# Kernel tuning notes

Measured on AMD Instinct MI355X. Metric: run time of the kernel, lower is better.

The kernel has to match this reference:

```python
import jax, jax.numpy as jnp
import numpy as np

N = 50000          # num_nodes
IN_CH = 128
H = 32             # hidden_channels
D = 2              # stalk dimension d (= final_d, add_lp=add_hp=False)
LAYERS = 4
EU = 400000        # undirected edges
E = 2 * EU         # directed edges (both orientations)
OUT = 32


def setup_inputs() -> dict:
    key = jax.random.key(0)
    ks = jax.random.split(key, 12)
    # undirected random graph; directed edge list holds both orientations so that
    # the reverse of directed edge e is e + EU (mod E)
    u = jax.random.randint(ks[0], (EU,), 0, N)
    v = jax.random.randint(ks[1], (EU,), 0, N)
    edge_index = jnp.stack([jnp.concatenate([u, v]), jnp.concatenate([v, u])]).astype(jnp.int64)
    x = jax.random.normal(ks[2], (N, IN_CH), dtype=jnp.float32)
    W1 = jax.random.normal(ks[3], (H * D, IN_CH), dtype=jnp.float32) / np.sqrt(IN_CH)
    b1 = jax.random.normal(ks[4], (H * D,), dtype=jnp.float32) * 0.01
    W_sheaf = jax.random.normal(ks[5], (LAYERS, D, 2 * D * H), dtype=jnp.float32) / np.sqrt(2 * D * H)
    # lin_left initialised to identity in the module; keep near-identity
    W_left = jnp.tile(jnp.eye(D, dtype=jnp.float32), (LAYERS, 1, 1)) \
        + 0.01 * jax.random.normal(ks[6], (LAYERS, D, D), dtype=jnp.float32)
    W_right = jax.random.normal(ks[7], (LAYERS, H, H), dtype=jnp.float32) / np.sqrt(H)
    eps = jnp.zeros((LAYERS, D, 1), dtype=jnp.float32) + 0.01 * jax.random.normal(ks[8], (LAYERS, D, 1), dtype=jnp.float32)
    W2 = jax.random.normal(ks[9], (OUT, D * H), dtype=jnp.float32) / np.sqrt(D * H)
    b2 = jax.random.normal(ks[10], (OUT,), dtype=jnp.float32) * 0.01
    return {"x": x, "edge_index": edge_index, "W1": W1, "b1": b1, "W_sheaf": W_sheaf,
            "W_left": W_left, "W_right": W_right, "eps": eps, "W2": W2, "b2": b2}


def reference(x, edge_index, W1, b1, W_sheaf, W_left, W_right, eps, W2, b2):
    # eval mode: dropouts are no-ops; diagnostic energies/eigsh omitted (no effect on output)
    n = x.shape[0]
    d = W_left.shape[-1]
    h = W_right.shape[-1]
    src, dst = edge_index[0], edge_index[1]
    e = src.shape[0]
    rev = (jnp.arange(e) + e // 2) % e  # reverse directed edge

    x = jax.nn.elu(x @ W1.T + b1)      # [N, d*h]
    x = x.reshape(n * d, h)
    x0 = x

    for l in range(W_left.shape[0]):
        # --- sheaf learner: tanh(Linear([x_i || x_j])), diag maps F: [E, d] ---
        xn = x.reshape(n, d * h)
        feat = jnp.concatenate([xn[src], xn[dst]], axis=-1)   # [E, 2dh]
        F = jnp.tanh(feat @ W_sheaf[l].T)                     # [E, d]
        Fr = F[rev]
        # --- diag sheaf Laplacian (normalised, augmented: D_hat = D + I) ---
        Dg = jax.ops.segment_sum(F * F, src, num_segments=n)  # [N, d] diagonal blocks
        dinv = jax.lax.rsqrt(Dg + 1.0)
        diagw = Dg * dinv * dinv                              # [N, d]
        offw = -F * Fr * dinv[src] * dinv[dst]                # [E, d]
        # --- left weights: view x^T as [h, N, d], mix stalk dim ---
        xt = x.T.reshape(h, n, d) @ W_left[l].T
        x = xt.reshape(h, n * d).T
        # --- right weights ---
        x = x @ W_right[l].T
        # --- spmm: y = L x ---
        x3 = x.reshape(n, d, h)
        y = diagw[:, :, None] * x3 \
            + jax.ops.segment_sum(offw[:, :, None] * x3[dst], src, num_segments=n)
        x = jax.nn.elu(y.reshape(n * d, h))
        # --- epsilon-gated residual ---
        coeff = jnp.tile(1.0 + jnp.tanh(eps[l]), (n, 1))      # [N*d, 1]
        x0 = coeff * x0 - x
        x = x0

    return x.reshape(n, d * h) @ W2.T + b2
```

## Files before the change

kernel.cpp:

```cpp
#include <hip/hip_runtime.h>
#include <math.h>

#define INCH 128
#define DH 64
#define H  32
#define D  2
#define LAYERS 4
#define OUTC 32

typedef __fp16 half4 __attribute__((ext_vector_type(4)));
typedef __fp16 half8 __attribute__((ext_vector_type(8)));
typedef float  f32x4 __attribute__((ext_vector_type(4)));

__device__ __forceinline__ float eluf(float v) { return v > 0.f ? v : expm1f(v); }

__device__ __forceinline__ float ftanh(float x) {
    float xc = fminf(9.0f, fmaxf(-9.0f, x));
    float e2 = __builtin_amdgcn_exp2f(xc * 2.885390081777927f);
    return (e2 - 1.0f) * __builtin_amdgcn_rcpf(e2 + 1.0f);
}

__global__ void k_prep(const float* __restrict__ W1, const float* __restrict__ W2,
                       const float* __restrict__ Wleft, const float* __restrict__ Wright,
                       __fp16* __restrict__ W1h, __fp16* __restrict__ W2h,
                       __fp16* __restrict__ Mlrh) {
    int idx = blockIdx.x * blockDim.x + threadIdx.x;
    if (idx < DH * INCH) {
        W1h[idx] = (__fp16)W1[idx];
    } else if (idx < DH * INCH + OUTC * DH) {
        int i = idx - DH * INCH;
        W2h[i] = (__fp16)W2[i];
    } else if (idx < DH * INCH + OUTC * DH + LAYERS * DH * DH) {
        int i = idx - DH * INCH - OUTC * DH;
        int l = i >> 12;
        int r = i & 4095;
        int row = r >> 6;
        int col = r & 63;
        int sp = row >> 5, c = row & 31;
        int s  = col >> 5, cp = col & 31;
        Mlrh[i] = (__fp16)(Wleft[l * 4 + sp * 2 + s] * Wright[l * 1024 + c * 32 + cp]);
    }
}

__global__ void k_hist(const int* __restrict__ src, int* __restrict__ deg, int E) {
    int e = blockIdx.x * blockDim.x + threadIdx.x;
    if (e < E) atomicAdd(&deg[src[e]], 1);
}

__global__ void k_bsum(const int* __restrict__ deg, int* __restrict__ bsum, int N) {
    int b = blockIdx.x, t = threadIdx.x;
    int lane = t & 63, wid = t >> 6;
    int base = b * 1024 + t * 4;
    int s = 0;
    #pragma unroll
    for (int i = 0; i < 4; ++i) {
        int idx = base + i;
        if (idx < N) s += deg[idx];
    }
    #pragma unroll
    for (int ofs = 32; ofs; ofs >>= 1) s += __shfl_xor(s, ofs);
    __shared__ int ws[4];
    if (lane == 0) ws[wid] = s;
    __syncthreads();
    if (t == 0) bsum[b] = ws[0] + ws[1] + ws[2] + ws[3];
}

__global__ void k_scan_small(int* __restrict__ bsum, int B) {
    int lane = threadIdx.x;
    int carry = 0;
    for (int base = 0; base < B; base += 64) {
        int i = base + lane;
        int v = (i < B) ? bsum[i] : 0;
        int incl = v;
        #pragma unroll
        for (int ofs = 1; ofs < 64; ofs <<= 1) {
            int tt = __shfl_up(incl, ofs);
            if (lane >= ofs) incl += tt;
        }
        if (i < B) bsum[i] = carry + incl - v;
        carry += __shfl(incl, 63);
    }
}

__global__ void k_scan_final(const int* __restrict__ deg, const int* __restrict__ bsum,
                             int* __restrict__ rowptr, int* __restrict__ cur, int N) {
    int b = blockIdx.x, t = threadIdx.x;
    int lane = t & 63, wid = t >> 6;
    int base = b * 1024 + t * 4;
    int v[4];
    int s = 0;
    #pragma unroll
    for (int i = 0; i < 4; ++i) {
        int idx = base + i;
        v[i] = (idx < N) ? deg[idx] : 0;
        s += v[i];
    }
    int incl = s;
    #pragma unroll
    for (int ofs = 1; ofs < 64; ofs <<= 1) {
        int tt = __shfl_up(incl, ofs);
        if (lane >= ofs) incl += tt;
    }
    __shared__ int ws[4];
    if (lane == 63) ws[wid] = incl;
    __syncthreads();
    int woff = 0;
    for (int k = 0; k < wid; ++k) woff += ws[k];
    int excl = bsum[b] + woff + incl - s;
    #pragma unroll
    for (int i = 0; i < 4; ++i) {
        int idx = base + i;
        if (idx < N) { rowptr[idx] = excl; cur[idx] = excl; }
        excl += v[i];
        if (idx == N - 1) rowptr[N] = excl;
    }
}

__global__ void k_scatter(const int* __restrict__ src, const int* __restrict__ dst,
                          int* __restrict__ cur, unsigned short* __restrict__ csr_dst, int E) {
    int e = blockIdx.x * blockDim.x + threadIdx.x;
    if (e >= E) return;
    int pos = atomicAdd(&cur[src[e]], 1);
    csr_dst[pos] = (unsigned short)dst[e];
}


__global__ __launch_bounds__(256) void k_mlp1_pq(const float* __restrict__ xin,
                                                 const __fp16* __restrict__ W1h,
                                                 const float* __restrict__ b1,
                                                 const float* __restrict__ Ws0,
                                                 float* __restrict__ X,
                                                 __fp16* __restrict__ NDh, int N) {
    __shared__ float xs[16 * INCH];
    __shared__ __fp16 wsh[DH * 132];
    __shared__ float xout[16 * DH];
    int t = threadIdx.x;
    int node0 = blockIdx.x * 16;
    for (int i = t; i < 16 * INCH / 4; i += 256) {
        int r = i >> 5, c = (i & 31) * 4;
        int node = node0 + r;
        f32x4 v = (node < N) ? __builtin_nontemporal_load((const f32x4*)(xin + (size_t)node * INCH + c))
                             : (f32x4){0.f, 0.f, 0.f, 0.f};
        *(f32x4*)&xs[r * INCH + c] = v;
    }
    for (int i = t; i < DH * INCH / 4; i += 256) {
        int r = i >> 5, c = (i & 31) * 4;
        *(uint2*)&wsh[r * 132 + c] = ((const uint2*)W1h)[i];
    }
    __syncthreads();
    int w = t >> 6, lane = t & 63;
    int oc0 = w * 16;
    int rr = lane & 15, g = lane >> 4;
    f32x4 acc = {0.f, 0.f, 0.f, 0.f};
    #pragma unroll
    for (int ks = 0; ks < INCH / 16; ++ks) {
        f32x4 xv = *(const f32x4*)&xs[rr * INCH + ks * 16 + g * 4];
        half4 af = {(__fp16)xv.x, (__fp16)xv.y, (__fp16)xv.z, (__fp16)xv.w};
        half4 bf = *(const half4*)&wsh[(oc0 + rr) * 132 + ks * 16 + g * 4];
        acc = __builtin_amdgcn_mfma_f32_16x16x16f16(af, bf, acc, 0, 0, 0);
    }
    int oc = oc0 + rr;
    float bb = b1[oc];
    #pragma unroll
    for (int r = 0; r < 4; ++r) {
        int node = node0 + g * 4 + r;
        float v = eluf(acc[r] + bb);
        xout[(g * 4 + r) * DH + oc] = v;
        if (node < N) X[(size_t)node * DH + oc] = v;
    }
    __syncthreads();
    float wsa = Ws0[lane];
    float wsb = Ws0[64 + lane];
    float wsc = Ws0[128 + lane];
    float wsd = Ws0[192 + lane];
    #pragma unroll
    for (int j = 0; j < 4; ++j) {
        int nl = w * 4 + j;
        int node = node0 + nl;
        float x = xout[nl * DH + lane];
        float p0 = x * wsa, q0 = x * wsb, p1 = x * wsc, q1 = x * wsd;
        #pragma unroll
        for (int ofs = 32; ofs; ofs >>= 1) {
            p0 += __shfl_xor(p0, ofs);
            q0 += __shfl_xor(q0, ofs);
            p1 += __shfl_xor(p1, ofs);
            q1 += __shfl_xor(q1, ofs);
        }
        if (lane == 0 && node < N) {
            half4 pq = {(__fp16)p0, (__fp16)p1, (__fp16)q0, (__fp16)q1};
            *(half4*)(NDh + (size_t)node * 8) = pq;
        }
    }
}

__global__ __launch_bounds__(256) void k_dglr(__fp16* __restrict__ NDh,
                                              const int* __restrict__ rowptr,
                                              const unsigned short* __restrict__ csr_dst,
                                              const float* __restrict__ X,
                                              const __fp16* __restrict__ Mlrh_l,
                                              __fp16* __restrict__ XW0h,
                                              __fp16* __restrict__ XW1h,
                                              int Bdg, int N) {
    __shared__ float xs[16 * DH];
    __shared__ __fp16 mlh[DH * 68];
    if (blockIdx.x < Bdg) {
        int lane = threadIdx.x & 63;
        int widl = threadIdx.x >> 6;
        int nn = lane >> 4, sub = lane & 15;
        int node = blockIdx.x * 16 + widl * 4 + nn;
        if (node >= N) return;
        half4 pqu = *(const half4*)(NDh + (size_t)node * 8);
        float pu0 = (float)pqu[0], pu1 = (float)pqu[1];
        int pos = rowptr[node], end = rowptr[node + 1];
        float sx = 0.f, sy = 0.f;
        for (int i = pos + sub; i < end; i += 16) {
            int v = (int)__builtin_nontemporal_load(csr_dst + i);
            half4 pqv = *(const half4*)(NDh + (size_t)v * 8);
            float fx = ftanh(pu0 + (float)pqv[2]);
            float fy = ftanh(pu1 + (float)pqv[3]);
            sx += fx * fx;
            sy += fy * fy;
        }
        #pragma unroll
        for (int ofs = 8; ofs; ofs >>= 1) {
            sx += __shfl_xor(sx, ofs);
            sy += __shfl_xor(sy, ofs);
        }
        if (sub == 0) {
            float i0 = 1.f / (sx + 1.f), i1 = 1.f / (sy + 1.f);
            half4 gi = {(__fp16)sqrtf(i0), (__fp16)sqrtf(i1), (__fp16)(sx * i0), (__fp16)(sy * i1)};
            *(half4*)(NDh + (size_t)node * 8 + 4) = gi;
        }
        return;
    }
    int t = threadIdx.x;
    int node0 = (blockIdx.x - Bdg) * 16;
    for (int i = t; i < 16 * DH / 4; i += 256) {
        int r = i >> 4, c = (i & 15) * 4;
        int node = node0 + r;
        f32x4 v = (node < N) ? __builtin_nontemporal_load((const f32x4*)(X + (size_t)node * DH + c))
                             : (f32x4){0.f, 0.f, 0.f, 0.f};
        *(f32x4*)&xs[r * DH + c] = v;
    }
    for (int i = t; i < DH * DH / 4; i += 256) {
        int r = i >> 4, c = (i & 15) * 4;
        *(uint2*)&mlh[r * 68 + c] = ((const uint2*)Mlrh_l)[i];
    }
    __syncthreads();
    int w = t >> 6, lane = t & 63;
    int oc0 = w * 16;
    int rr = lane & 15, g = lane >> 4;
    f32x4 acc = {0.f, 0.f, 0.f, 0.f};
    #pragma unroll
    for (int ks = 0; ks < DH / 16; ++ks) {
        f32x4 xv = *(const f32x4*)&xs[rr * DH + ks * 16 + g * 4];
        half4 af = {(__fp16)xv.x, (__fp16)xv.y, (__fp16)xv.z, (__fp16)xv.w};
        half4 bf = *(const half4*)&mlh[(oc0 + rr) * 68 + ks * 16 + g * 4];
        acc = __builtin_amdgcn_mfma_f32_16x16x16f16(af, bf, acc, 0, 0, 0);
    }
    int oc = oc0 + rr;
    int sp = oc >> 5, c = oc & 31;
    __fp16* __restrict__ XWs = sp ? XW1h : XW0h;
    #pragma unroll
    for (int r = 0; r < 4; ++r) {
        int node = node0 + g * 4 + r;
        if (node < N) XWs[(size_t)node * H + c] = (__fp16)acc[r];
    }
}

__global__ __launch_bounds__(256) void k_out(const float* __restrict__ X,
                                             const __fp16* __restrict__ W2h,
                                             const float* __restrict__ b2,
                                             float* __restrict__ out, int N) {
    __shared__ float xs[32 * DH];
    __shared__ __fp16 w2s[OUTC * 68];
    int t = threadIdx.x;
    int node0 = blockIdx.x * 32;
    for (int i = t; i < 32 * DH / 4; i += 256) {
        int r = i >> 4, c = (i & 15) * 4;
        int node = node0 + r;
        f32x4 v = (node < N) ? __builtin_nontemporal_load((const f32x4*)(X + (size_t)node * DH + c))
                             : (f32x4){0.f, 0.f, 0.f, 0.f};
        *(f32x4*)&xs[r * DH + c] = v;
    }
    for (int i = t; i < OUTC * DH / 4; i += 256) {
        int r = i >> 4, c = (i & 15) * 4;
        *(uint2*)&w2s[r * 68 + c] = ((const uint2*)W2h)[i];
    }
    __syncthreads();
    int w = t >> 6, lane = t & 63;
    int nt = w >> 1;
    int oc0 = (w & 1) * 16;
    int rr = lane & 15, g = lane >> 4;
    f32x4 acc = {0.f, 0.f, 0.f, 0.f};
    #pragma unroll
    for (int ks = 0; ks < DH / 16; ++ks) {
        f32x4 xv = *(const f32x4*)&xs[(nt * 16 + rr) * DH + ks * 16 + g * 4];
        half4 af = {(__fp16)xv.x, (__fp16)xv.y, (__fp16)xv.z, (__fp16)xv.w};
        half4 bf = *(const half4*)&w2s[(oc0 + rr) * 68 + ks * 16 + g * 4];
        acc = __builtin_amdgcn_mfma_f32_16x16x16f16(af, bf, acc, 0, 0, 0);
    }
    int oc = oc0 + rr;
    float bb = b2[oc];
    #pragma unroll
    for (int r = 0; r < 4; ++r) {
        int node = node0 + nt * 16 + g * 4 + r;
        if (node < N) out[(size_t)node * OUTC + oc] = acc[r] + bb;
    }
}

__global__ void k_spmm_fin_pq(const __fp16* __restrict__ XW0h, const __fp16* __restrict__ XW1h,
                              const __fp16* __restrict__ NDh, const int* __restrict__ rowptr,
                              const unsigned short* __restrict__ csr_dst,
                              const float* __restrict__ eps_l, const float* __restrict__ Wsn,
                              float* __restrict__ X, __fp16* __restrict__ NDhn, int N) {
    int wid = (blockIdx.x * blockDim.x + threadIdx.x) >> 6;
    int lane = threadIdx.x & 63;
    if (wid >= N) return;
    int q = lane >> 3;
    int m = lane & 7;
    half8 ndu = *(const half8*)(NDh + (size_t)wid * 8);
    float pu0 = (float)ndu[0], pu1 = (float)ndu[1];
    float qu0 = (float)ndu[2], qu1 = (float)ndu[3];
    float dinv0 = (float)ndu[4], dinv1 = (float)ndu[5];
    int pos = rowptr[wid], end = rowptr[wid + 1];

    float a0x = 0.f, a0y = 0.f, a0z = 0.f, a0w = 0.f;
    float a1x = 0.f, a1y = 0.f, a1z = 0.f, a1w = 0.f;

    for (int chunk = pos; chunk < end; chunk += 64) {
        int myidx = chunk + lane;
        int dmy = 0;
        float w0my = 0.f, w1my = 0.f;
        if (myidx < end) {
            dmy = (int)__builtin_nontemporal_load(csr_dst + myidx);
            half8 ndd = *(const half8*)(NDh + (size_t)dmy * 8);
            float ff0 = ftanh(pu0 + (float)ndd[2]), fb0 = ftanh((float)ndd[0] + qu0);
            float ff1 = ftanh(pu1 + (float)ndd[3]), fb1 = ftanh((float)ndd[1] + qu1);
            w0my = -ff0 * fb0 * dinv0 * (float)ndd[4];
            w1my = -ff1 * fb1 * dinv1 * (float)ndd[5];
        }
        int lim = end - chunk; if (lim > 64) lim = 64;
        for (int b = 0; b < lim; b += 8) {
            int sl = b + q;
            int d      = __shfl(dmy, sl);
            float w0e  = __shfl(w0my, sl);
            float w1e  = __shfl(w1my, sl);
            half4 g0 = *(const half4*)(XW0h + (size_t)d * H + m * 4);
            half4 g1 = *(const half4*)(XW1h + (size_t)d * H + m * 4);
            a0x += w0e * (float)g0.x; a0y += w0e * (float)g0.y;
            a0z += w0e * (float)g0.z; a0w += w0e * (float)g0.w;
            a1x += w1e * (float)g1.x; a1y += w1e * (float)g1.y;
            a1z += w1e * (float)g1.z; a1w += w1e * (float)g1.w;
        }
    }
    #pragma unroll
    for (int ofs = 8; ofs <= 32; ofs <<= 1) {
        a0x += __shfl_xor(a0x, ofs); a0y += __shfl_xor(a0y, ofs);
        a0z += __shfl_xor(a0z, ofs); a0w += __shfl_xor(a0w, ofs);
        a1x += __shfl_xor(a1x, ofs); a1y += __shfl_xor(a1y, ofs);
        a1z += __shfl_xor(a1z, ofs); a1w += __shfl_xor(a1w, ofs);
    }
    if (q == 0) {
        float diag0 = (float)ndu[6];
        float diag1 = (float)ndu[7];
        half4 xw0 = *(const half4*)(XW0h + (size_t)wid * H + m * 4);
        half4 xw1 = *(const half4*)(XW1h + (size_t)wid * H + m * 4);
        size_t b0 = (size_t)wid * DH + m * 4;
        size_t b1 = b0 + 32;
        float coeff0 = 1.f + tanhf(eps_l[0]);
        float coeff1 = 1.f + tanhf(eps_l[1]);
        f32x4 xo0 = __builtin_nontemporal_load((const f32x4*)(X + b0));
        f32x4 xo1 = __builtin_nontemporal_load((const f32x4*)(X + b1));
        f32x4 xn0, xn1;
        xn0.x = coeff0 * xo0.x - eluf(diag0 * (float)xw0.x + a0x);
        xn0.y = coeff0 * xo0.y - eluf(diag0 * (float)xw0.y + a0y);
        xn0.z = coeff0 * xo0.z - eluf(diag0 * (float)xw0.z + a0z);
        xn0.w = coeff0 * xo0.w - eluf(diag0 * (float)xw0.w + a0w);
        xn1.x = coeff1 * xo1.x - eluf(diag1 * (float)xw1.x + a1x);
        xn1.y = coeff1 * xo1.y - eluf(diag1 * (float)xw1.y + a1y);
        xn1.z = coeff1 * xo1.z - eluf(diag1 * (float)xw1.z + a1z);
        xn1.w = coeff1 * xo1.w - eluf(diag1 * (float)xw1.w + a1w);
        __builtin_nontemporal_store(xn0, (f32x4*)(X + b0));
        __builtin_nontemporal_store(xn1, (f32x4*)(X + b1));
        if (Wsn) {
            f32x4 wa0 = *(const f32x4*)(Wsn + m * 4);
            f32x4 wa1 = *(const f32x4*)(Wsn + 32 + m * 4);
            f32x4 wb0 = *(const f32x4*)(Wsn + 64 + m * 4);
            f32x4 wb1 = *(const f32x4*)(Wsn + 96 + m * 4);
            f32x4 wc0 = *(const f32x4*)(Wsn + 128 + m * 4);
            f32x4 wc1 = *(const f32x4*)(Wsn + 160 + m * 4);
            f32x4 wd0 = *(const f32x4*)(Wsn + 192 + m * 4);
            f32x4 wd1 = *(const f32x4*)(Wsn + 224 + m * 4);
            float p0 = xn0.x * wa0.x + xn0.y * wa0.y + xn0.z * wa0.z + xn0.w * wa0.w
                     + xn1.x * wa1.x + xn1.y * wa1.y + xn1.z * wa1.z + xn1.w * wa1.w;
            float q0 = xn0.x * wb0.x + xn0.y * wb0.y + xn0.z * wb0.z + xn0.w * wb0.w
                     + xn1.x * wb1.x + xn1.y * wb1.y + xn1.z * wb1.z + xn1.w * wb1.w;
            float p1 = xn0.x * wc0.x + xn0.y * wc0.y + xn0.z * wc0.z + xn0.w * wc0.w
                     + xn1.x * wc1.x + xn1.y * wc1.y + xn1.z * wc1.z + xn1.w * wc1.w;
            float q1 = xn0.x * wd0.x + xn0.y * wd0.y + xn0.z * wd0.z + xn0.w * wd0.w
                     + xn1.x * wd1.x + xn1.y * wd1.y + xn1.z * wd1.z + xn1.w * wd1.w;
            #pragma unroll
            for (int ofs = 1; ofs < 8; ofs <<= 1) {
                p0 += __shfl_xor(p0, ofs);
                q0 += __shfl_xor(q0, ofs);
                p1 += __shfl_xor(p1, ofs);
                q1 += __shfl_xor(q1, ofs);
            }
            if (m == 0) {
                half4 pq = {(__fp16)p0, (__fp16)p1, (__fp16)q0, (__fp16)q1};
                *(half4*)(NDhn + (size_t)wid * 8) = pq;
            }
        }
    }
}

extern "C" void kernel_launch(void* const* d_in, const int* in_sizes, int n_in,
                              void* d_out, int out_size, void* d_ws, size_t ws_size,
                              hipStream_t stream) {
    const float* xin    = (const float*)d_in[0];
    const int*   ei     = (const int*)d_in[1];
    const float* W1     = (const float*)d_in[2];
    const float* b1     = (const float*)d_in[3];
    const float* Wsheaf = (const float*)d_in[4];
    const float* Wleft  = (const float*)d_in[5];
    const float* Wright = (const float*)d_in[6];
    const float* eps    = (const float*)d_in[7];
    const float* W2     = (const float*)d_in[8];
    const float* b2     = (const float*)d_in[9];
    float* out = (float*)d_out;

    int N = in_sizes[0] / INCH;
    int E = in_sizes[1] / 2;
    const int* src = ei;
    const int* dst = ei + E;

    size_t off = 0;
    auto alloc = [&](size_t nbytes) {
        char* p = (char*)d_ws + off;
        off += (nbytes + 255) & ~(size_t)255;
        return p;
    };
    float*          X       = (float*)alloc((size_t)N * DH * 4);
    __fp16*         XW0h    = (__fp16*)alloc((size_t)N * H * 2);
    __fp16*         XW1h    = (__fp16*)alloc((size_t)N * H * 2);
    __fp16*         NDha    = (__fp16*)alloc((size_t)N * 16);
    __fp16*         NDhb    = (__fp16*)alloc((size_t)N * 16);
    int*            deg     = (int*)alloc((size_t)N * 4);
    int*            rowptr  = (int*)alloc(((size_t)N + 1) * 4);
    int*            cur     = (int*)alloc((size_t)N * 4);
    unsigned short* csr_dst = (unsigned short*)alloc((size_t)E * 2);
    int*            bsum    = (int*)alloc(4096);
    __fp16*         W1h     = (__fp16*)alloc((size_t)DH * INCH * 2);
    __fp16*         W2h     = (__fp16*)alloc((size_t)OUTC * DH * 2);
    __fp16*         Mlrh    = (__fp16*)alloc((size_t)LAYERS * DH * DH * 2);

    int B = (N + 1023) / 1024;

    int prep_total = DH * INCH + OUTC * DH + LAYERS * DH * DH;
    k_prep<<<(prep_total + 255) / 256, 256, 0, stream>>>(W1, W2, Wleft, Wright, W1h, W2h, Mlrh);
    hipMemsetAsync(deg, 0, (size_t)N * sizeof(int), stream);
    k_hist<<<(E + 255) / 256, 256, 0, stream>>>(src, deg, E);
    k_bsum<<<B, 256, 0, stream>>>(deg, bsum, N);
    k_scan_small<<<1, 64, 0, stream>>>(bsum, B);
    k_scan_final<<<B, 256, 0, stream>>>(deg, bsum, rowptr, cur, N);
    k_scatter<<<(E + 255) / 256, 256, 0, stream>>>(src, dst, cur, csr_dst, E);

    k_mlp1_pq<<<(N + 15) / 16, 256, 0, stream>>>(xin, W1h, b1, Wsheaf, X, NDha, N);

    __fp16* NDcur = NDha;
    __fp16* NDnext = NDhb;
    int Bdg = (N + 15) / 16;
    int Blr = (N + 15) / 16;
    for (int l = 0; l < LAYERS; ++l) {
        k_dglr<<<Bdg + Blr, 256, 0, stream>>>(NDcur, rowptr, csr_dst, X,
                                              Mlrh + (size_t)l * DH * DH, XW0h, XW1h, Bdg, N);
        const float* Wsn = (l + 1 < LAYERS) ? (Wsheaf + (l + 1) * 2 * INCH) : nullptr;
        k_spmm_fin_pq<<<(N + 3) / 4, 256, 0, stream>>>(XW0h, XW1h, NDcur, rowptr, csr_dst,
                                                       eps + l * 2, Wsn, X, NDnext, N);
        __fp16* tmp = NDcur; NDcur = NDnext; NDnext = tmp;
    }

    k_out<<<(N + 31) / 32, 256, 0, stream>>>(X, W2h, b2, out, N);
}
```

Baseline: 378.4 us.

## Split SpMM per node across two waves, one per stalk dimension

Each node is now handled by two wavefronts, one per stalk component, where before a single wave covered both. Each wave gathers only one XW half and computes one edge weight, which halves per-wave register use and doubles the number of waves in flight for the latency-bound gather. The two partial p/q projections are combined through shared memory after a block barrier. In exchange, edge indices and neighbor metadata are loaded twice and the final step pays a barrier.

```diff
diff --git a/kernel.cpp b/kernel.cpp
--- a/kernel.cpp
+++ b/kernel.cpp
@@ -309,97 +309,79 @@
     }
 }
 
-__global__ void k_spmm_fin_pq(const __fp16* __restrict__ XW0h, const __fp16* __restrict__ XW1h,
-                              const __fp16* __restrict__ NDh, const int* __restrict__ rowptr,
-                              const unsigned short* __restrict__ csr_dst,
-                              const float* __restrict__ eps_l, const float* __restrict__ Wsn,
-                              float* __restrict__ X, __fp16* __restrict__ NDhn, int N) {
-    int wid = (blockIdx.x * blockDim.x + threadIdx.x) >> 6;
+__global__ __launch_bounds__(256) void k_spmm_fin_pq(
+        const __fp16* __restrict__ XW0h, const __fp16* __restrict__ XW1h,
+        const __fp16* __restrict__ NDh, const int* __restrict__ rowptr,
+        const unsigned short* __restrict__ csr_dst,
+        const float* __restrict__ eps_l, const float* __restrict__ Wsn,
+        float* __restrict__ X, __fp16* __restrict__ NDhn, int N) {
+    __shared__ float4 pq_lds[2][2];
+    int wvl = threadIdx.x >> 6;
+    int nl  = wvl >> 1;
+    int st  = wvl & 1;
     int lane = threadIdx.x & 63;
-    if (wid >= N) return;
+    int wid = blockIdx.x * 2 + nl;
+    bool active = wid < N;
     int q = lane >> 3;
     int m = lane & 7;
-    half8 ndu = *(const half8*)(NDh + (size_t)wid * 8);
-    float pu0 = (float)ndu[0], pu1 = (float)ndu[1];
-    float qu0 = (float)ndu[2], qu1 = (float)ndu[3];
-    float dinv0 = (float)ndu[4], dinv1 = (float)ndu[5];
-    int pos = rowptr[wid], end = rowptr[wid + 1];
-
-    float a0x = 0.f, a0y = 0.f, a0z = 0.f, a0w = 0.f;
-    float a1x = 0.f, a1y = 0.f, a1z = 0.f, a1w = 0.f;
-
+    const __fp16* __restrict__ XWh = st ? XW1h : XW0h;
+
+    float pu = 0.f, qu = 0.f, dinv = 0.f, diag = 0.f;
+    int pos = 0, end = 0;
+    if (active) {
+        half8 ndu = *(const half8*)(NDh + (size_t)wid * 8);
+        pu = (float)ndu[st]; qu = (float)ndu[2 + st];
+        dinv = (float)ndu[4 + st]; diag = (float)ndu[6 + st];
+        pos = rowptr[wid]; end = rowptr[wid + 1];
+    }
+
+    float ax = 0.f, ay = 0.f, az = 0.f, aw = 0.f;
     for (int chunk = pos; chunk < end; chunk += 64) {
         int myidx = chunk + lane;
         int dmy = 0;
-        float w0my = 0.f, w1my = 0.f;
+        float wmy = 0.f;
         if (myidx < end) {
             dmy = (int)__builtin_nontemporal_load(csr_dst + myidx);
             half8 ndd = *(const half8*)(NDh + (size_t)dmy * 8);
-            float ff0 = ftanh(pu0 + (float)ndd[2]), fb0 = ftanh((float)ndd[0] + qu0);
-            float ff1 = ftanh(pu1 + (float)ndd[3]), fb1 = ftanh((float)ndd[1] + qu1);
-            w0my = -ff0 * fb0 * dinv0 * (float)ndd[4];
-            w1my = -ff1 * fb1 * dinv1 * (float)ndd[5];
+            wmy = -ftanh(pu + (float)ndd[2 + st]) * ftanh((float)ndd[st] + qu)
+                  * dinv * (float)ndd[4 + st];
         }
         int lim = end - chunk; if (lim > 64) lim = 64;
         for (int b = 0; b < lim; b += 8) {
             int sl = b + q;
-            int d      = __shfl(dmy, sl);
-            float w0e  = __shfl(w0my, sl);
-            float w1e  = __shfl(w1my, sl);
-            half4 g0 = *(const half4*)(XW0h + (size_t)d * H + m * 4);
-            half4 g1 = *(const half4*)(XW1h + (size_t)d * H + m * 4);
-            a0x += w0e * (float)g0.x; a0y += w0e * (float)g0.y;
-            a0z += w0e * (float)g0.z; a0w += w0e * (float)g0.w;
-            a1x += w1e * (float)g1.x; a1y += w1e * (float)g1.y;
-            a1z += w1e * (float)g1.z; a1w += w1e * (float)g1.w;
+            int d     = __shfl(dmy, sl);
+            float wgt = __shfl(wmy, sl);
+            half4 g = *(const half4*)(XWh + (size_t)d * H + m * 4);
+            ax += wgt * (float)g.x; ay += wgt * (float)g.y;
+            az += wgt * (float)g.z; aw += wgt * (float)g.w;
         }
     }
     #pragma unroll
     for (int ofs = 8; ofs <= 32; ofs <<= 1) {
-        a0x += __shfl_xor(a0x, ofs); a0y += __shfl_xor(a0y, ofs);
-        a0z += __shfl_xor(a0z, ofs); a0w += __shfl_xor(a0w, ofs);
-        a1x += __shfl_xor(a1x, ofs); a1y += __shfl_xor(a1y, ofs);
-        a1z += __shfl_xor(a1z, ofs); a1w += __shfl_xor(a1w, ofs);
-    }
-    if (q == 0) {
-        float diag0 = (float)ndu[6];
-        float diag1 = (float)ndu[7];
-        half4 xw0 = *(const half4*)(XW0h + (size_t)wid * H + m * 4);
-        half4 xw1 = *(const half4*)(XW1h + (size_t)wid * H + m * 4);
-        size_t b0 = (size_t)wid * DH + m * 4;
-        size_t b1 = b0 + 32;
-        float coeff0 = 1.f + tanhf(eps_l[0]);
-        float coeff1 = 1.f + tanhf(eps_l[1]);
-        f32x4 xo0 = __builtin_nontemporal_load((const f32x4*)(X + b0));
-        f32x4 xo1 = __builtin_nontemporal_load((const f32x4*)(X + b1));
-        f32x4 xn0, xn1;
-        xn0.x = coeff0 * xo0.x - eluf(diag0 * (float)xw0.x + a0x);
-        xn0.y = coeff0 * xo0.y - eluf(diag0 * (float)xw0.y + a0y);
-        xn0.z = coeff0 * xo0.z - eluf(diag0 * (float)xw0.z + a0z);
-        xn0.w = coeff0 * xo0.w - eluf(diag0 * (float)xw0.w + a0w);
-        xn1.x = coeff1 * xo1.x - eluf(diag1 * (float)xw1.x + a1x);
-        xn1.y = coeff1 * xo1.y - eluf(diag1 * (float)xw1.y + a1y);
-        xn1.z = coeff1 * xo1.z - eluf(diag1 * (float)xw1.z + a1z);
-        xn1.w = coeff1 * xo1.w - eluf(diag1 * (float)xw1.w + a1w);
-        __builtin_nontemporal_store(xn0, (f32x4*)(X + b0));
-        __builtin_nontemporal_store(xn1, (f32x4*)(X + b1));
+        ax += __shfl_xor(ax, ofs); ay += __shfl_xor(ay, ofs);
+        az += __shfl_xor(az, ofs); aw += __shfl_xor(aw, ofs);
+    }
+    if (active && q == 0) {
+        half4 xw = *(const half4*)(XWh + (size_t)wid * H + m * 4);
+        size_t bx = (size_t)wid * DH + st * 32 + m * 4;
+        float coeff = 1.f + tanhf(eps_l[st]);
+        f32x4 xo = __builtin_nontemporal_load((const f32x4*)(X + bx));
+        f32x4 xn;
+        xn.x = coeff * xo.x - eluf(diag * (float)xw.x + ax);
+        xn.y = coeff * xo.y - eluf(diag * (float)xw.y + ay);
+        xn.z = coeff * xo.z - eluf(diag * (float)xw.z + az);
+        xn.w = coeff * xo.w - eluf(diag * (float)xw.w + aw);
+        __builtin_nontemporal_store(xn, (f32x4*)(X + bx));
         if (Wsn) {
-            f32x4 wa0 = *(const f32x4*)(Wsn + m * 4);
-            f32x4 wa1 = *(const f32x4*)(Wsn + 32 + m * 4);
-            f32x4 wb0 = *(const f32x4*)(Wsn + 64 + m * 4);
-            f32x4 wb1 = *(const f32x4*)(Wsn + 96 + m * 4);
-            f32x4 wc0 = *(const f32x4*)(Wsn + 128 + m * 4);
-            f32x4 wc1 = *(const f32x4*)(Wsn + 160 + m * 4);
-            f32x4 wd0 = *(const f32x4*)(Wsn + 192 + m * 4);
-            f32x4 wd1 = *(const f32x4*)(Wsn + 224 + m * 4);
-            float p0 = xn0.x * wa0.x + xn0.y * wa0.y + xn0.z * wa0.z + xn0.w * wa0.w
-                     + xn1.x * wa1.x + xn1.y * wa1.y + xn1.z * wa1.z + xn1.w * wa1.w;
-            float q0 = xn0.x * wb0.x + xn0.y * wb0.y + xn0.z * wb0.z + xn0.w * wb0.w
-                     + xn1.x * wb1.x + xn1.y * wb1.y + xn1.z * wb1.z + xn1.w * wb1.w;
-            float p1 = xn0.x * wc0.x + xn0.y * wc0.y + xn0.z * wc0.z + xn0.w * wc0.w
-                     + xn1.x * wc1.x + xn1.y * wc1.y + xn1.z * wc1.z + xn1.w * wc1.w;
-            float q1 = xn0.x * wd0.x + xn0.y * wd0.y + xn0.z * wd0.z + xn0.w * wd0.w
-                     + xn1.x * wd1.x + xn1.y * wd1.y + xn1.z * wd1.z + xn1.w * wd1.w;
+            int coffs = st * 32 + m * 4;
+            f32x4 wpa = *(const f32x4*)(Wsn + coffs);
+            f32x4 wqa = *(const f32x4*)(Wsn + 64 + coffs);
+            f32x4 wpb = *(const f32x4*)(Wsn + 128 + coffs);
+            f32x4 wqb = *(const f32x4*)(Wsn + 192 + coffs);
+            float p0 = xn.x * wpa.x + xn.y * wpa.y + xn.z * wpa.z + xn.w * wpa.w;
+            float q0 = xn.x * wqa.x + xn.y * wqa.y + xn.z * wqa.z + xn.w * wqa.w;
+            float p1 = xn.x * wpb.x + xn.y * wpb.y + xn.z * wpb.z + xn.w * wpb.w;
+            float q1 = xn.x * wqb.x + xn.y * wqb.y + xn.z * wqb.z + xn.w * wqb.w;
             #pragma unroll
             for (int ofs = 1; ofs < 8; ofs <<= 1) {
                 p0 += __shfl_xor(p0, ofs);
@@ -407,10 +389,17 @@
                 p1 += __shfl_xor(p1, ofs);
                 q1 += __shfl_xor(q1, ofs);
             }
-            if (m == 0) {
-                half4 pq = {(__fp16)p0, (__fp16)p1, (__fp16)q0, (__fp16)q1};
-                *(half4*)(NDhn + (size_t)wid * 8) = pq;
-            }
+            if (m == 0) pq_lds[nl][st] = make_float4(p0, p1, q0, q1);
+        }
+    }
+    if (Wsn) {
+        __syncthreads();
+        if (active && st == 0 && lane == 0) {
+            float4 a = pq_lds[nl][0];
+            float4 b = pq_lds[nl][1];
+            half4 pq = {(__fp16)(a.x + b.x), (__fp16)(a.y + b.y),
+                        (__fp16)(a.z + b.z), (__fp16)(a.w + b.w)};
+            *(half4*)(NDhn + (size_t)wid * 8) = pq;
         }
     }
 }
@@ -476,7 +465,7 @@
         k_dglr<<<Bdg + Blr, 256, 0, stream>>>(NDcur, rowptr, csr_dst, X,
                                               Mlrh + (size_t)l * DH * DH, XW0h, XW1h, Bdg, N);
         const float* Wsn = (l + 1 < LAYERS) ? (Wsheaf + (l + 1) * 2 * INCH) : nullptr;
-        k_spmm_fin_pq<<<(N + 3) / 4, 256, 0, stream>>>(XW0h, XW1h, NDcur, rowptr, csr_dst,
+        k_spmm_fin_pq<<<(N + 1) / 2, 256, 0, stream>>>(XW0h, XW1h, NDcur, rowptr, csr_dst,
                                                        eps + l * 2, Wsn, X, NDnext, N);
         __fp16* tmp = NDcur; NDcur = NDnext; NDnext = tmp;
     }
```

After: 469.9 us. 1.24x slower.
